# Kernel optimization log

Measured on AMD Instinct MI355X. Metric: run time of the kernel, lower is better.

The kernel has to match this reference:

```python
import jax, jax.numpy as jnp
import numpy as np

B, S, DIM = 128, 256, 512          # batch, grid tokens (16*16), input feature dim
D = 128                             # embedding_dim
K = 16384                           # num_embeddings
GH = GW = 16                        # grid size
EPS = 1e-12


def setup_inputs() -> dict:
    key = jax.random.key(0)
    ks = jax.random.split(key, 10)
    return {
        "input_data_first": jax.random.normal(ks[0], (B, S, DIM), jnp.float32),
        "input_data_last": jax.random.normal(ks[1], (B, S, DIM), jnp.float32),
        "random_vector": jax.random.normal(ks[2], (B * 64, D), jnp.float32),
        "codebooks": jax.random.normal(ks[3], (K, D), jnp.float32),
        "W_in": jax.random.normal(ks[4], (DIM, D), jnp.float32) / np.sqrt(DIM),
        "b_in": jnp.zeros((D,), jnp.float32),
        "conv_w": jax.random.normal(ks[5], (D, D, 3, 3), jnp.float32) / np.sqrt(D * 9),
        "conv_b": jnp.zeros((D,), jnp.float32),
        "W_out": jax.random.normal(ks[6], (D, DIM), jnp.float32) / np.sqrt(D),
        "b_out": jnp.zeros((DIM,), jnp.float32),
        "codebooks_used": jnp.zeros((K,), jnp.int32),
    }


def _encode(x, W_in, b_in, conv_w, conv_b):
    h = x @ W_in + b_in                                  # [B,S,D]
    h = jnp.transpose(h, (0, 2, 1)).reshape(B, D, GH, GW)  # [B,D,16,16]
    h = jax.lax.conv_general_dilated(
        h, conv_w, window_strides=(2, 2), padding=[(1, 1), (1, 1)],
        dimension_numbers=("NCHW", "OIHW", "NCHW"))
    h = h + conv_b[None, :, None, None]                  # [B,D,8,8]
    h = h.reshape(B, D, -1)                              # [B,D,64]
    h = jnp.transpose(h, (0, 2, 1)).reshape(-1, D)       # [B*64, D]
    return h


def reference(input_data_first, input_data_last, random_vector, codebooks,
              W_in, b_in, conv_w, conv_b, W_out, b_out, codebooks_used):
    e_first = _encode(input_data_first, W_in, b_in, conv_w, conv_b)
    e_last = _encode(input_data_last, W_in, b_in, conv_w, conv_b)
    x = e_last - e_first                                 # [N,D]

    # squared-distance to every codebook entry: [N,K]
    dists = (jnp.sum(x * x, axis=1, keepdims=True)
             - 2.0 * (x @ codebooks.T)
             + jnp.sum(codebooks * codebooks, axis=1)[None, :])
    min_indices = jnp.argmin(dists, axis=1)              # [N]
    hard_q = codebooks[min_indices]                      # [N,D]

    norm_res = jnp.sqrt(jnp.sum((x - hard_q) ** 2, axis=1, keepdims=True))
    norm_rnd = jnp.sqrt(jnp.sum(random_vector ** 2, axis=1, keepdims=True))
    vq_error = (norm_res / norm_rnd + EPS) * random_vector
    quantized = x + vq_error                             # [N,D]

    counts = jnp.zeros((K,), jnp.float32).at[min_indices].add(1.0)
    avg_probs = counts / x.shape[0]
    perplexity = jnp.exp(-jnp.sum(avg_probs * jnp.log(avg_probs + EPS)))

    new_used = codebooks_used + counts.astype(jnp.int32)

    # decode (faithful to torch: raw memory reinterpretation, not inverse transpose)
    q = quantized.reshape(B, D, -1)                      # [B,D,64]
    q = jnp.transpose(q, (0, 2, 1))                      # [B,64,D]
    out = q @ W_out + b_out                              # [B,64,DIM]
    return out, perplexity, new_used, min_indices.reshape(B, -1)
```

## Files before the change

### kernel.cpp

```cpp
#include <hip/hip_runtime.h>
#include <math.h>

#define NROWS 8192
#define KCB   16384

using frag_ab = __attribute__((ext_vector_type(8))) short;
using frag_cd = __attribute__((ext_vector_type(4))) float;
using f32x4   = __attribute__((ext_vector_type(4))) float;
using f64x4   = __attribute__((ext_vector_type(4))) double;

__device__ inline unsigned short f2bf(float f) {
    unsigned u = __float_as_uint(f);
    return (unsigned short)((u + 0x7FFFu + ((u >> 16) & 1u)) >> 16);
}

__global__ __launch_bounds__(256) void k_wt(const float* __restrict__ cw,
                                            float* __restrict__ W2) {
    int gid = blockIdx.x * 256 + threadIdx.x;
    if (gid >= 147456) return;
    int co = gid & 127;
    int ci = (gid >> 7) & 127;
    int kk = gid >> 14;
    W2[gid] = cw[(size_t)co * 1152 + ci * 9 + kk];
}

__global__ __launch_bounds__(256) void k_c2(const float* __restrict__ cb,
                                            float* __restrict__ c2f) {
    int k = blockIdx.x * 256 + threadIdx.x;
    const float* row = cb + (size_t)k * 128;
    double s = 0.0;
    #pragma unroll
    for (int d = 0; d < 128; d += 4) {
        float4 v = *(const float4*)(row + d);
        s += (double)v.x * v.x + (double)v.y * v.y
           + (double)v.z * v.z + (double)v.w * v.w;
    }
    c2f[k] = (float)s + 1024.0f;
}

__global__ __launch_bounds__(256) void k_cbbf(const float* __restrict__ cb,
                                              unsigned short* __restrict__ Cbb) {
    int gid = blockIdx.x * 256 + threadIdx.x;
    float4 v = ((const float4*)cb)[gid];
    ushort4 o;
    o.x = f2bf(v.x); o.y = f2bf(v.y); o.z = f2bf(v.z); o.w = f2bf(v.w);
    ((ushort4*)Cbb)[gid] = o;
}

__global__ __launch_bounds__(256) void k_encode_gemm(
    const float* __restrict__ last, const float* __restrict__ first,
    const float* __restrict__ W_in, double* __restrict__ H)
{
    __shared__ double As[32][66];
    __shared__ double Bs[32][132];
    const int tid  = threadIdx.x;
    const int lane = tid & 63;
    const int w    = tid >> 6;
    const int row0 = blockIdx.x * 64;
    const int wm   = (w & 1) * 32;
    const int wn   = (w >> 1) * 64;
    const int lm   = lane & 15;
    const int kq   = lane >> 4;

    f64x4 z; z[0] = 0.0; z[1] = 0.0; z[2] = 0.0; z[3] = 0.0;
    const double dl = (double)lane;
    f64x4 d1 = __builtin_amdgcn_mfma_f64_16x16x4f64(dl, 1.0, z, 0, 0, 0);
    f64x4 d2 = __builtin_amdgcn_mfma_f64_16x16x4f64(1.0, dl, z, 0, 0, 0);
    const double pk = (double)(1 << (4 * kq));
    f64x4 d3 = __builtin_amdgcn_mfma_f64_16x16x4f64(pk, dl, z, 0, 0, 0);
    int pm[4], pn[4];
    int okl = 1;
    #pragma unroll
    for (int s = 0; s < 4; ++s) {
        double v1 = d1[s] - 96.0, v2 = d2[s] - 96.0;
        int i1 = (int)v1, i2 = (int)v2;
        okl &= (d1[s] == (double)(96 + i1)) & (i1 >= 0) & (i1 < 64) & ((i1 & 3) == 0);
        okl &= (d2[s] == (double)(96 + i2)) & (i2 >= 0) & (i2 < 64) & ((i2 & 3) == 0);
        pm[s] = i1 >> 2;
        pn[s] = i2 >> 2;
        okl &= (d3[s] == 4369.0 * (double)pn[s] + 205056.0);
    }
    const int ok = __all(okl);
    if (!ok) {
        #pragma unroll
        for (int s = 0; s < 4; ++s) { pm[s] = 4 * kq + s; pn[s] = lm; }
    }

    f64x4 acc[2][4];
    #pragma unroll
    for (int i = 0; i < 2; ++i)
        #pragma unroll
        for (int j = 0; j < 4; ++j)
            #pragma unroll
            for (int q = 0; q < 4; ++q) acc[i][j][q] = 0.0;

    const int ar = tid >> 2;
    const int ak = (tid & 3) * 8;
    const int bkk = tid >> 3;
    const int bc  = (tid & 7) * 16;

    for (int k0 = 0; k0 < 512; k0 += 32) {
        if (k0) __syncthreads();
        {
            const float* lp = last  + (size_t)(row0 + ar) * 512 + k0 + ak;
            const float* fp = first + (size_t)(row0 + ar) * 512 + k0 + ak;
            const float4 l0 = *(const float4*)(lp);
            const float4 l1 = *(const float4*)(lp + 4);
            const float4 f0 = *(const float4*)(fp);
            const float4 f1 = *(const float4*)(fp + 4);
            As[ak + 0][ar] = (double)l0.x - (double)f0.x;
            As[ak + 1][ar] = (double)l0.y - (double)f0.y;
            As[ak + 2][ar] = (double)l0.z - (double)f0.z;
            As[ak + 3][ar] = (double)l0.w - (double)f0.w;
            As[ak + 4][ar] = (double)l1.x - (double)f1.x;
            As[ak + 5][ar] = (double)l1.y - (double)f1.y;
            As[ak + 6][ar] = (double)l1.z - (double)f1.z;
            As[ak + 7][ar] = (double)l1.w - (double)f1.w;
        }
        {
            const float* wp = W_in + (size_t)(k0 + bkk) * 128 + bc;
            #pragma unroll
            for (int q = 0; q < 4; ++q) {
                const float4 b4 = *(const float4*)(wp + 4 * q);
                Bs[bkk][bc + 4 * q + 0] = (double)b4.x;
                Bs[bkk][bc + 4 * q + 1] = (double)b4.y;
                Bs[bkk][bc + 4 * q + 2] = (double)b4.z;
                Bs[bkk][bc + 4 * q + 3] = (double)b4.w;
            }
        }
        __syncthreads();
        if (ok) {
            #pragma unroll
            for (int kc = 0; kc < 8; ++kc) {
                const int kk = kc * 4 + kq;
                double a0 = As[kk][wm + lm];
                double a1 = As[kk][wm + 16 + lm];
                double b0 = Bs[kk][wn + lm];
                double b1 = Bs[kk][wn + 16 + lm];
                double b2 = Bs[kk][wn + 32 + lm];
                double b3 = Bs[kk][wn + 48 + lm];
                acc[0][0] = __builtin_amdgcn_mfma_f64_16x16x4f64(a0, b0, acc[0][0], 0, 0, 0);
                acc[0][1] = __builtin_amdgcn_mfma_f64_16x16x4f64(a0, b1, acc[0][1], 0, 0, 0);
                acc[0][2] = __builtin_amdgcn_mfma_f64_16x16x4f64(a0, b2, acc[0][2], 0, 0, 0);
                acc[0][3] = __builtin_amdgcn_mfma_f64_16x16x4f64(a0, b3, acc[0][3], 0, 0, 0);
                acc[1][0] = __builtin_amdgcn_mfma_f64_16x16x4f64(a1, b0, acc[1][0], 0, 0, 0);
                acc[1][1] = __builtin_amdgcn_mfma_f64_16x16x4f64(a1, b1, acc[1][1], 0, 0, 0);
                acc[1][2] = __builtin_amdgcn_mfma_f64_16x16x4f64(a1, b2, acc[1][2], 0, 0, 0);
                acc[1][3] = __builtin_amdgcn_mfma_f64_16x16x4f64(a1, b3, acc[1][3], 0, 0, 0);
            }
        } else {
            #pragma unroll 4
            for (int k = 0; k < 32; ++k) {
                double b0 = Bs[k][wn + lm];
                double b1 = Bs[k][wn + 16 + lm];
                double b2 = Bs[k][wn + 32 + lm];
                double b3 = Bs[k][wn + 48 + lm];
                #pragma unroll
                for (int i = 0; i < 2; ++i) {
                    const double* ap = &As[k][wm + i * 16 + 4 * kq];
                    #pragma unroll
                    for (int s = 0; s < 4; ++s) {
                        double a = ap[s];
                        acc[i][0][s] = fma(a, b0, acc[i][0][s]);
                        acc[i][1][s] = fma(a, b1, acc[i][1][s]);
                        acc[i][2][s] = fma(a, b2, acc[i][2][s]);
                        acc[i][3][s] = fma(a, b3, acc[i][3][s]);
                    }
                }
            }
        }
    }
    #pragma unroll
    for (int i = 0; i < 2; ++i)
        #pragma unroll
        for (int j = 0; j < 4; ++j)
            #pragma unroll
            for (int s = 0; s < 4; ++s)
                H[(size_t)(row0 + wm + i * 16 + pm[s]) * 128 + wn + j * 16 + pn[s]]
                    = acc[i][j][s];
}

__global__ __launch_bounds__(256) void k_conv(
    const double* __restrict__ H, const float* __restrict__ W2,
    double* __restrict__ X, unsigned short* __restrict__ Xb)
{
    __shared__ double Hs[3 * 16 * 128];
    const int b   = blockIdx.x >> 3;
    const int oh  = blockIdx.x & 7;
    const int tid = threadIdx.x;
    const int ih0 = 2 * oh - 1;
    for (int it = 0; it < 24; ++it) {
        int idx = it * 256 + tid;
        int r = idx >> 11;
        int rem = idx & 2047;
        int ih = ih0 + r;
        Hs[idx] = (ih >= 0) ? H[(size_t)b * 32768 + (size_t)ih * 2048 + rem] : 0.0;
    }
    __syncthreads();
    const int co   = tid & 127;
    const int half = tid >> 7;
    const int iwb  = half * 8 - 1;
    double acc[4] = {0, 0, 0, 0};
    for (int ci = 0; ci < 128; ++ci) {
        #pragma unroll
        for (int kh = 0; kh < 3; ++kh) {
            double in[9];
            #pragma unroll
            for (int t = 0; t < 9; ++t) {
                int iw = iwb + t;
                in[t] = (iw >= 0) ? Hs[kh * 2048 + iw * 128 + ci] : 0.0;
            }
            #pragma unroll
            for (int kw = 0; kw < 3; ++kw) {
                double w = (double)W2[(size_t)((kh * 3 + kw) * 128 + ci) * 128 + co];
                #pragma unroll
                for (int i = 0; i < 4; ++i)
                    acc[i] = fma(in[2 * i + kw], w, acc[i]);
            }
        }
    }
    #pragma unroll
    for (int i = 0; i < 4; ++i) {
        int ow = half * 4 + i;
        size_t n = (size_t)b * 64 + oh * 8 + ow;
        X [n * 128 + co] = acc[i];
        Xb[n * 128 + co] = f2bf((float)acc[i]);
    }
}

__global__ __launch_bounds__(256) void k_dist_mfma(
    const unsigned short* __restrict__ Xb, const unsigned short* __restrict__ Cbb,
    const float* __restrict__ c2f, int* __restrict__ cand)
{
    __shared__ __align__(16) unsigned short Xs[128 * 128];
    __shared__ __align__(16) unsigned short Cs[128 * 128];
    const int tid   = threadIdx.x;
    const int row0  = blockIdx.x * 128;
    const int split = blockIdx.y;
    const int lane  = tid & 63;
    const int w     = tid >> 6;
    const int quad  = lane >> 4;
    const int lm    = lane & 15;
    const int cw    = (w & 1) * 64;
    const int rw    = (w >> 1) * 64;

    #pragma unroll
    for (int it = 0; it < 8; ++it) {
        int flat = it * 256 + tid;
        int r = flat >> 4, ch = flat & 15;
        *(uint4*)&Xs[r * 128 + (((ch ^ r) & 15) << 3) + (ch & 16 ? 0 : 0)] =
            *(const uint4*)(Xb + (size_t)(row0 + r) * 128 + ch * 8);
    }

    unsigned k1[4], k2[4];
    #pragma unroll
    for (int j = 0; j < 4; ++j) { k1[j] = 0xFFFFFFFFu; k2[j] = 0xFFFFFFFFu; }

    for (int chunk = 0; chunk < 16; ++chunk) {
        const int kb = split * 2048 + chunk * 128;
        if (chunk) __syncthreads();
        #pragma unroll
        for (int it = 0; it < 8; ++it) {
            int flat = it * 256 + tid;
            int r = flat >> 4, ch = flat & 15;
            *(uint4*)&Cs[r * 128 + ((ch ^ (r & 15)) << 3)] =
                *(const uint4*)(Cbb + (size_t)(kb + r) * 128 + ch * 8);
        }
        __syncthreads();

        frag_cd acc[4][4];
        #pragma unroll
        for (int i = 0; i < 4; ++i)
            #pragma unroll
            for (int j = 0; j < 4; ++j)
                #pragma unroll
                for (int r = 0; r < 4; ++r) acc[i][j][r] = 0.f;

        #pragma unroll
        for (int kk = 0; kk < 4; ++kk) {
            const int chs = ((kk * 4 + quad) ^ lm) << 3;
            frag_ab a[4], b[4];
            #pragma unroll
            for (int i = 0; i < 4; ++i)
                a[i] = *(const frag_ab*)&Cs[(cw + i * 16 + lm) * 128 + chs];
            #pragma unroll
            for (int j = 0; j < 4; ++j)
                b[j] = *(const frag_ab*)&Xs[(rw + j * 16 + lm) * 128 + chs];
            #pragma unroll
            for (int i = 0; i < 4; ++i)
                #pragma unroll
                for (int j = 0; j < 4; ++j)
                    acc[i][j] = __builtin_amdgcn_mfma_f32_16x16x32_bf16(
                        a[i], b[j], acc[i][j], 0, 0, 0);
        }

        const int ib = chunk * 128 + cw + quad * 4;
        #pragma unroll
        for (int i = 0; i < 4; ++i) {
            f32x4 c2v = *(const f32x4*)(c2f + kb + cw + i * 16 + quad * 4);
            #pragma unroll
            for (int j = 0; j < 4; ++j) {
                #pragma unroll
                for (int r = 0; r < 4; ++r) {
                    float u = fmaf(-2.f, acc[i][j][r], c2v[r]);
                    unsigned key = (__float_as_uint(u) & 0xFFFFF800u)
                                 | (unsigned)(ib + i * 16 + r);
                    unsigned nk1 = min(key, k1[j]);
                    k2[j] = min(max(key, k1[j]), k2[j]);
                    k1[j] = nk1;
                }
            }
        }
    }

    __syncthreads();
    uint2* kred = (uint2*)Cs;
    #pragma unroll
    for (int j = 0; j < 4; ++j)
        kred[(rw + j * 16 + lm) * 8 + (w & 1) * 4 + quad] = make_uint2(k1[j], k2[j]);
    __syncthreads();
    if (tid < 128) {
        unsigned b1 = 0xFFFFFFFFu, b2 = 0xFFFFFFFFu;
        for (int e = 0; e < 8; ++e) {
            uint2 kv = kred[tid * 8 + e];
            unsigned n1 = min(kv.x, b1); b2 = min(max(kv.x, b1), b2); b1 = n1;
            n1 = min(kv.y, b1);          b2 = min(max(kv.y, b1), b2); b1 = n1;
        }
        int base = split * 2048;
        int* o = cand + (size_t)(row0 + tid) * 16 + split * 2;
        o[0] = base + (int)(b1 & 0x7FFu);
        o[1] = base + (int)(b2 & 0x7FFu);
    }
}

__global__ __launch_bounds__(256) void k_refine(
    const double* __restrict__ X, const float* __restrict__ cb,
    const int* __restrict__ cand, const float* __restrict__ rnd,
    int* __restrict__ counts, float* __restrict__ quant,
    float* __restrict__ out_mi)
{
    const int wid  = threadIdx.x >> 6;
    const int lane = threadIdx.x & 63;
    const int row  = blockIdx.x * 4 + wid;
    const double x0 = X[(size_t)row * 128 + lane];
    const double x1 = X[(size_t)row * 128 + 64 + lane];
    double bestv = 1e300; int bestk = 0;
    for (int c = 0; c < 16; ++c) {
        int k = cand[(size_t)row * 16 + c] & (KCB - 1);
        double t0 = x0 - (double)cb[(size_t)k * 128 + lane];
        double t1 = x1 - (double)cb[(size_t)k * 128 + 64 + lane];
        double s = t0 * t0 + t1 * t1;
        #pragma unroll
        for (int off = 32; off > 0; off >>= 1) s += __shfl_xor(s, off, 64);
        if (s < bestv) { bestv = s; bestk = k; }
    }
    double r0 = (double)rnd[(size_t)row * 128 + lane];
    double r1 = (double)rnd[(size_t)row * 128 + 64 + lane];
    double rs = r0 * r0 + r1 * r1;
    #pragma unroll
    for (int off = 32; off > 0; off >>= 1) rs += __shfl_xor(rs, off, 64);
    double ratio = sqrt(bestv) / sqrt(rs) + 1e-12;
    quant[(size_t)row * 128 + lane]      = (float)(x0 + ratio * r0);
    quant[(size_t)row * 128 + 64 + lane] = (float)(x1 + ratio * r1);
    if (lane == 0) {
        out_mi[row] = (float)bestk;
        atomicAdd(counts + bestk, 1);
    }
}

__global__ __launch_bounds__(256) void k_perplex(
    const int* __restrict__ counts, const int* __restrict__ used_in,
    float* __restrict__ out_used, float* __restrict__ out_perp)
{
    __shared__ double red[256];
    int tid = threadIdx.x;
    double e = 0.0;
    for (int k = tid; k < KCB; k += 256) {
        int c = counts[k];
        out_used[k] = (float)(used_in[k] + c);
        if (c > 0) {
            double p = (double)c / 8192.0;
            e += p * log(p + 1e-12);
        }
    }
    red[tid] = e;
    __syncthreads();
    for (int s = 128; s > 0; s >>= 1) {
        if (tid < s) red[tid] += red[tid + s];
        __syncthreads();
    }
    if (tid == 0) out_perp[0] = (float)exp(-red[0]);
}

__global__ __launch_bounds__(256) void k_decode(
    const float* __restrict__ quant, const float* __restrict__ W_out,
    const float* __restrict__ b_out, float* __restrict__ out)
{
    __shared__ float As[8192];
    __shared__ float Bs[8192];
    const int tid = threadIdx.x;
    const int m0  = blockIdx.x * 64;
    const int b   = blockIdx.y;
    #pragma unroll
    for (int it = 0; it < 8; ++it) {
        int flat = it * 1024 + tid * 4;
        *(float4*)&As[flat] = *(const float4*)(quant + (size_t)b * 8192 + flat);
        int d2 = flat >> 6, m = flat & 63;
        *(float4*)&Bs[flat] = *(const float4*)(W_out + (size_t)d2 * 512 + m0 + m);
    }
    __syncthreads();
    const int tx = tid & 15, ty = tid >> 4;
    float acc[4][4];
    #pragma unroll
    for (int i = 0; i < 4; ++i)
        #pragma unroll
        for (int j = 0; j < 4; ++j) acc[i][j] = 0.f;
    #pragma unroll 8
    for (int d2 = 0; d2 < 128; ++d2) {
        float4 a  = *(const float4*)&As[d2 * 64 + ty * 4];
        float4 b4 = *(const float4*)&Bs[d2 * 64 + tx * 4];
        float av[4] = {a.x, a.y, a.z, a.w};
        float bv[4] = {b4.x, b4.y, b4.z, b4.w};
        #pragma unroll
        for (int i = 0; i < 4; ++i)
            #pragma unroll
            for (int j = 0; j < 4; ++j)
                acc[i][j] = fmaf(av[i], bv[j], acc[i][j]);
    }
    float4 bo = *(const float4*)(b_out + m0 + tx * 4);
    float bob[4] = {bo.x, bo.y, bo.z, bo.w};
    #pragma unroll
    for (int i = 0; i < 4; ++i) {
        int s2 = ty * 4 + i;
        float4 o;
        o.x = acc[i][0] + bob[0];
        o.y = acc[i][1] + bob[1];
        o.z = acc[i][2] + bob[2];
        o.w = acc[i][3] + bob[3];
        *(float4*)(out + (size_t)b * 32768 + (size_t)s2 * 512 + m0 + tx * 4) = o;
    }
}

extern "C" void kernel_launch(void* const* d_in, const int* in_sizes, int n_in,
                              void* d_out, int out_size, void* d_ws, size_t ws_size,
                              hipStream_t stream) {
    const float* first  = (const float*)d_in[0];
    const float* last   = (const float*)d_in[1];
    const float* rnd    = (const float*)d_in[2];
    const float* cb     = (const float*)d_in[3];
    const float* W_in   = (const float*)d_in[4];
    const float* conv_w = (const float*)d_in[6];
    const float* W_out  = (const float*)d_in[8];
    const float* b_out  = (const float*)d_in[9];
    const int*   used   = (const int*)d_in[10];

    float* out      = (float*)d_out;
    float* out_perp = out + 4194304;
    float* out_used = out + 4194305;
    float* out_mi   = out + 4194305 + 16384;

    char* ws = (char*)d_ws;
    double*         H      = (double*)(ws);
    double*         X      = (double*)(ws + 33554432);
    unsigned short* Cbb    = (unsigned short*)(ws + 41943040);
    float*          W2     = (float*) (ws + 46137344);
    float*          c2f    = (float*) (ws + 46727168);
    int*            cand   = (int*)   (ws + 46792704);
    float*          quant  = (float*) (ws + 47316992);
    int*            counts = (int*)   (ws + 51511296);
    unsigned short* Xb     = (unsigned short*)(ws + 51576832);

    hipMemsetAsync(counts, 0, KCB * sizeof(int), stream);
    k_wt<<<576, 256, 0, stream>>>(conv_w, W2);
    k_c2<<<64, 256, 0, stream>>>(cb, c2f);
    k_cbbf<<<2048, 256, 0, stream>>>(cb, Cbb);
    k_encode_gemm<<<512, 256, 0, stream>>>(last, first, W_in, H);
    k_conv<<<1024, 256, 0, stream>>>(H, W2, X, Xb);
    k_dist_mfma<<<dim3(64, 8), 256, 0, stream>>>(Xb, Cbb, c2f, cand);
    k_refine<<<2048, 256, 0, stream>>>(X, cb, cand, rnd, counts, quant, out_mi);
    k_perplex<<<1, 256, 0, stream>>>(counts, used, out_used, out_perp);
    k_decode<<<dim3(8, 128), 256, 0, stream>>>(quant, W_out, b_out, out);
}
```

Before: 504.2 us.

## Run strided conv on FP64 MFMA with 16-output-row tiles per block

The 3x3 stride-2 convolution kernel is rewritten to compute each block's 16 output positions by 128 channels with FP64 16x16x4 MFMA instructions, replacing per-thread scalar FMA loops. The block tiling is changed from one output row per block to two output rows per block (512 blocks), staging five input rows in shared memory with vectorized double2 loads. The MFMA lane-layout probe is factored into a shared helper, and a scalar fallback is kept for the case where the probe fails. Weights are read directly from global memory per MFMA step, and the larger shared buffer may reduce occupancy.

```diff
diff --git a/kernel.cpp b/kernel.cpp
--- a/kernel.cpp
+++ b/kernel.cpp
@@ -12,6 +12,27 @@
 __device__ inline unsigned short f2bf(float f) {
     unsigned u = __float_as_uint(f);
     return (unsigned short)((u + 0x7FFFu + ((u >> 16) & 1u)) >> 16);
+}
+
+__device__ inline int mfma_f64_probe(int pm[4], int pn[4], int kq) {
+    f64x4 z; z[0] = 0.0; z[1] = 0.0; z[2] = 0.0; z[3] = 0.0;
+    const double dl = (double)(threadIdx.x & 63);
+    f64x4 d1 = __builtin_amdgcn_mfma_f64_16x16x4f64(dl, 1.0, z, 0, 0, 0);
+    f64x4 d2 = __builtin_amdgcn_mfma_f64_16x16x4f64(1.0, dl, z, 0, 0, 0);
+    const double pk = (double)(1 << (4 * kq));
+    f64x4 d3 = __builtin_amdgcn_mfma_f64_16x16x4f64(pk, dl, z, 0, 0, 0);
+    int okl = 1;
+    #pragma unroll
+    for (int s = 0; s < 4; ++s) {
+        double v1 = d1[s] - 96.0, v2 = d2[s] - 96.0;
+        int i1 = (int)v1, i2 = (int)v2;
+        okl &= (d1[s] == (double)(96 + i1)) & (i1 >= 0) & (i1 < 64) & ((i1 & 3) == 0);
+        okl &= (d2[s] == (double)(96 + i2)) & (i2 >= 0) & (i2 < 64) & ((i2 & 3) == 0);
+        pm[s] = i1 >> 2;
+        pn[s] = i2 >> 2;
+        okl &= (d3[s] == 4369.0 * (double)pn[s] + 205056.0);
+    }
+    return __all(okl);
 }
 
 __global__ __launch_bounds__(256) void k_wt(const float* __restrict__ cw,
@@ -62,25 +83,8 @@
     const int lm   = lane & 15;
     const int kq   = lane >> 4;
 
-    f64x4 z; z[0] = 0.0; z[1] = 0.0; z[2] = 0.0; z[3] = 0.0;
-    const double dl = (double)lane;
-    f64x4 d1 = __builtin_amdgcn_mfma_f64_16x16x4f64(dl, 1.0, z, 0, 0, 0);
-    f64x4 d2 = __builtin_amdgcn_mfma_f64_16x16x4f64(1.0, dl, z, 0, 0, 0);
-    const double pk = (double)(1 << (4 * kq));
-    f64x4 d3 = __builtin_amdgcn_mfma_f64_16x16x4f64(pk, dl, z, 0, 0, 0);
     int pm[4], pn[4];
-    int okl = 1;
-    #pragma unroll
-    for (int s = 0; s < 4; ++s) {
-        double v1 = d1[s] - 96.0, v2 = d2[s] - 96.0;
-        int i1 = (int)v1, i2 = (int)v2;
-        okl &= (d1[s] == (double)(96 + i1)) & (i1 >= 0) & (i1 < 64) & ((i1 & 3) == 0);
-        okl &= (d2[s] == (double)(96 + i2)) & (i2 >= 0) & (i2 < 64) & ((i2 & 3) == 0);
-        pm[s] = i1 >> 2;
-        pn[s] = i2 >> 2;
-        okl &= (d3[s] == 4369.0 * (double)pn[s] + 205056.0);
-    }
-    const int ok = __all(okl);
+    const int ok = mfma_f64_probe(pm, pn, kq);
     if (!ok) {
         #pragma unroll
         for (int s = 0; s < 4; ++s) { pm[s] = 4 * kq + s; pn[s] = lm; }
@@ -184,47 +188,99 @@
     const double* __restrict__ H, const float* __restrict__ W2,
     double* __restrict__ X, unsigned short* __restrict__ Xb)
 {
-    __shared__ double Hs[3 * 16 * 128];
-    const int b   = blockIdx.x >> 3;
-    const int oh  = blockIdx.x & 7;
-    const int tid = threadIdx.x;
-    const int ih0 = 2 * oh - 1;
-    for (int it = 0; it < 24; ++it) {
-        int idx = it * 256 + tid;
-        int r = idx >> 11;
-        int rem = idx & 2047;
-        int ih = ih0 + r;
-        Hs[idx] = (ih >= 0) ? H[(size_t)b * 32768 + (size_t)ih * 2048 + rem] : 0.0;
+    __shared__ double Hs[5 * 2048];
+    const int tid  = threadIdx.x;
+    const int lane = tid & 63;
+    const int w    = tid >> 6;
+    const int n0   = blockIdx.x * 16;
+    const int b    = blockIdx.x >> 2;
+    const int j    = blockIdx.x & 3;
+    const int ihbase = 4 * j - 1;
+    const int wn   = w * 32;
+    const int lm   = lane & 15;
+    const int kq   = lane >> 4;
+
+    int pm[4], pn[4];
+    const int ok = mfma_f64_probe(pm, pn, kq);
+
+    #pragma unroll
+    for (int it = 0; it < 20; ++it) {
+        int slot = it * 256 + tid;
+        int r = slot >> 10;
+        int rem = (slot & 1023) * 2;
+        int ih = ihbase + r;
+        double2 v = (ih >= 0)
+            ? *(const double2*)(H + (size_t)b * 32768 + (size_t)ih * 2048 + rem)
+            : make_double2(0.0, 0.0);
+        *(double2*)&Hs[r * 2048 + rem] = v;
     }
     __syncthreads();
-    const int co   = tid & 127;
-    const int half = tid >> 7;
-    const int iwb  = half * 8 - 1;
-    double acc[4] = {0, 0, 0, 0};
-    for (int ci = 0; ci < 128; ++ci) {
+
+    if (ok) {
+        f64x4 acc0, acc1;
+        #pragma unroll
+        for (int q = 0; q < 4; ++q) { acc0[q] = 0.0; acc1[q] = 0.0; }
+        const int ow = lm & 7, ohl = lm >> 3;
         #pragma unroll
         for (int kh = 0; kh < 3; ++kh) {
-            double in[9];
-            #pragma unroll
-            for (int t = 0; t < 9; ++t) {
-                int iw = iwb + t;
-                in[t] = (iw >= 0) ? Hs[kh * 2048 + iw * 128 + ci] : 0.0;
+            #pragma unroll
+            for (int kw = 0; kw < 3; ++kw) {
+                const int tap = kh * 3 + kw;
+                const int iw  = 2 * ow - 1 + kw;
+                const int ihr = 2 * ohl + kh;
+                const int valid = (iw >= 0) & (ihbase + ihr >= 0);
+                const int aoff = valid ? (ihr * 2048 + iw * 128 + kq) : 0;
+                const double msk = valid ? 1.0 : 0.0;
+                const float* wbase = W2 + (size_t)(tap * 128 + kq) * 128 + wn + lm;
+                #pragma unroll 4
+                for (int ci0 = 0; ci0 < 128; ci0 += 4) {
+                    double a  = Hs[aoff + ci0] * msk;
+                    double b0 = (double)wbase[ci0 * 128];
+                    double b1 = (double)wbase[ci0 * 128 + 16];
+                    acc0 = __builtin_amdgcn_mfma_f64_16x16x4f64(a, b0, acc0, 0, 0, 0);
+                    acc1 = __builtin_amdgcn_mfma_f64_16x16x4f64(a, b1, acc1, 0, 0, 0);
+                }
             }
-            #pragma unroll
-            for (int kw = 0; kw < 3; ++kw) {
-                double w = (double)W2[(size_t)((kh * 3 + kw) * 128 + ci) * 128 + co];
+        }
+        #pragma unroll
+        for (int s = 0; s < 4; ++s) {
+            size_t n = n0 + pm[s];
+            int c0 = wn + pn[s];
+            X [n * 128 + c0]      = acc0[s];
+            Xb[n * 128 + c0]      = f2bf((float)acc0[s]);
+            X [n * 128 + c0 + 16] = acc1[s];
+            Xb[n * 128 + c0 + 16] = f2bf((float)acc1[s]);
+        }
+    } else {
+        const int co   = wn + (lane & 31);
+        const int half = lane >> 5;
+        double facc[8];
+        #pragma unroll
+        for (int i = 0; i < 8; ++i) facc[i] = 0.0;
+        for (int ci = 0; ci < 128; ++ci) {
+            #pragma unroll
+            for (int kh = 0; kh < 3; ++kh) {
                 #pragma unroll
-                for (int i = 0; i < 4; ++i)
-                    acc[i] = fma(in[2 * i + kw], w, acc[i]);
+                for (int kw = 0; kw < 3; ++kw) {
+                    double wv = (double)W2[(size_t)((kh * 3 + kw) * 128 + ci) * 128 + co];
+                    #pragma unroll
+                    for (int i = 0; i < 8; ++i) {
+                        int m = half * 8 + i;
+                        int iw = 2 * (m & 7) - 1 + kw;
+                        int ihr = 2 * (m >> 3) + kh;
+                        double hv = (iw >= 0 && ihbase + ihr >= 0)
+                                  ? Hs[ihr * 2048 + iw * 128 + ci] : 0.0;
+                        facc[i] = fma(hv, wv, facc[i]);
+                    }
+                }
             }
         }
-    }
-    #pragma unroll
-    for (int i = 0; i < 4; ++i) {
-        int ow = half * 4 + i;
-        size_t n = (size_t)b * 64 + oh * 8 + ow;
-        X [n * 128 + co] = acc[i];
-        Xb[n * 128 + co] = f2bf((float)acc[i]);
+        #pragma unroll
+        for (int i = 0; i < 8; ++i) {
+            size_t n = n0 + half * 8 + i;
+            X [n * 128 + co] = facc[i];
+            Xb[n * 128 + co] = f2bf((float)facc[i]);
+        }
     }
 }
 
@@ -475,7 +531,7 @@
     k_c2<<<64, 256, 0, stream>>>(cb, c2f);
     k_cbbf<<<2048, 256, 0, stream>>>(cb, Cbb);
     k_encode_gemm<<<512, 256, 0, stream>>>(last, first, W_in, H);
-    k_conv<<<1024, 256, 0, stream>>>(H, W2, X, Xb);
+    k_conv<<<512, 256, 0, stream>>>(H, W2, X, Xb);
     k_dist_mfma<<<dim3(64, 8), 256, 0, stream>>>(Xb, Cbb, c2f, cand);
     k_refine<<<2048, 256, 0, stream>>>(X, cb, cand, rnd, counts, quant, out_mi);
     k_perplex<<<1, 256, 0, stream>>>(counts, used, out_used, out_perp);
```

After: 456.5 us. 1.1x faster.
